# Performance work log

Hardware: AMD Instinct MI355X
Metric: run time of the kernel (lower is better)

Reference implementation:

```python
import jax, jax.numpy as jnp
import numpy as np

N_FEATURES = 7
N_SETS = 2
N_RULES = N_SETS ** N_FEATURES  # 128
BATCH = 65536


def setup_inputs() -> dict:
    key = jax.random.key(0)
    ks = jax.random.split(key, 7)
    centres = jnp.tile(jnp.linspace(-1.5, 1.5, N_SETS)[None, :], (N_FEATURES, 1))
    x = jax.random.normal(ks[0], (BATCH, N_FEATURES), jnp.float32)
    mu_gauss = centres + 0.1 * jax.random.normal(ks[1], centres.shape, jnp.float32)
    sigma_gauss = jnp.full((N_FEATURES, N_SETS), 0.8, jnp.float32)
    trap_a = centres - 1.2 + 0.05 * jax.random.normal(ks[2], centres.shape, jnp.float32)
    trap_b = centres - 0.4 + 0.05 * jax.random.normal(ks[3], centres.shape, jnp.float32)
    trap_c = centres + 0.4 + 0.05 * jax.random.normal(ks[4], centres.shape, jnp.float32)
    trap_d = centres + 1.2 + 0.05 * jax.random.normal(ks[5], centres.shape, jnp.float32)
    mf_mix = jnp.array(0.0, jnp.float32)
    t_norm_weight = jnp.array(0.0, jnp.float32)
    consequent = 0.01 * jax.random.normal(ks[6], (N_RULES, N_FEATURES + 1), jnp.float32)
    # itertools.product(range(S), repeat=F) ordering == np.indices row-major order
    rule_indices = jnp.asarray(
        np.indices((N_SETS,) * N_FEATURES).reshape(N_FEATURES, -1).T, jnp.int32
    )  # (N_RULES, N_FEATURES)
    return {
        "x": x, "mu_gauss": mu_gauss, "sigma_gauss": sigma_gauss,
        "trap_a": trap_a, "trap_b": trap_b, "trap_c": trap_c, "trap_d": trap_d,
        "mf_mix": mf_mix, "t_norm_weight": t_norm_weight,
        "consequent": consequent, "rule_indices": rule_indices,
    }


def reference(x, mu_gauss, sigma_gauss, trap_a, trap_b, trap_c, trap_d,
              mf_mix, t_norm_weight, consequent, rule_indices):
    B = x.shape[0]
    xe = x[..., None]  # (B, F, 1)
    # Gaussian MF
    sig = jnp.clip(sigma_gauss, 1e-6, None)
    gauss = jnp.exp(-(xe - mu_gauss) ** 2 / (2.0 * sig ** 2))  # (B, F, S)
    # Trapezoid MF with soft-sorted params a<b<=c<d
    params = jnp.sort(jnp.stack([trap_a, trap_b, trap_c, trap_d], axis=-1), axis=-1)
    a, b, c, d = params[..., 0], params[..., 1], params[..., 2], params[..., 3]
    left = jnp.clip((xe - a) / (b - a + 1e-6), 0.0, 1.0)
    flat = ((xe >= b) & (xe <= c)).astype(x.dtype)
    right = jnp.clip((d - xe) / (d - c + 1e-6), 0.0, 1.0)
    trap = jnp.maximum(jnp.minimum(left, right), flat)  # (B, F, S)
    # MF blend
    alpha = jax.nn.sigmoid(mf_mix)
    mem = alpha * gauss + (1.0 - alpha) * trap  # (B, F, S)
    # Rule gather: for each feature i, pick mem[:, i, rule_indices[:, i]]
    feat_idx = jnp.arange(N_FEATURES)[:, None]               # (F, 1)
    gathered = mem[:, feat_idx, rule_indices.T]              # (B, F, R)
    # Learnable t-norm: blend of product and min
    w = jax.nn.sigmoid(t_norm_weight)
    firing = w * jnp.prod(gathered, axis=1) + (1.0 - w) * jnp.min(gathered, axis=1)  # (B, R)
    norm_firing = firing / (jnp.sum(firing, axis=1, keepdims=True) + 1e-8)
    # TSK consequent: x_aug @ consequent^T
    x_aug = jnp.concatenate([jnp.ones((B, 1), x.dtype), x], axis=1)  # (B, F+1)
    rule_out = x_aug @ consequent.T                                  # (B, R)
    out = jnp.sum(norm_firing * rule_out, axis=1, keepdims=True)     # (B, 1)
    return (out, norm_firing, mem)
```

## Files before the change

### kernel.cpp

```cpp
#include <hip/hip_runtime.h>

#define NF 7
#define NR 128
#define ROWS 32

__global__ __launch_bounds__(256) void anfis_kernel(
    const float* __restrict__ x,
    const float* __restrict__ mu_g,  const float* __restrict__ sig_g,
    const float* __restrict__ ta, const float* __restrict__ tb,
    const float* __restrict__ tc, const float* __restrict__ td,
    const float* __restrict__ mf_mix, const float* __restrict__ tnw,
    const float* __restrict__ consequent,
    const int*   __restrict__ rule_idx,
    float* __restrict__ out,
    float* __restrict__ nf_out,
    float* __restrict__ mem_out,
    int nrows)
{
    __shared__ float s_x[ROWS][8];
    __shared__ float s_mem[ROWS][16];
    __shared__ unsigned int s_mask32[32];

    const int tid  = threadIdx.x;
    const int base = blockIdx.x * ROWS;

    if (tid < NR) {
        int m = 0;
        #pragma unroll
        for (int i = 0; i < NF; ++i)
            if (rule_idx[tid * NF + i] != 0) m |= (1 << i);
        ((unsigned char*)s_mask32)[tid] = (unsigned char)m;
    }

    const float alpha = 1.0f / (1.0f + __expf(-mf_mix[0]));
    const float w     = 1.0f / (1.0f + __expf(-tnw[0]));
    const float a1 = 1.0f - alpha, w1 = 1.0f - w;

    {
        const int j   = tid & 15;
        const int r16 = tid >> 4;

        float mu_j = 0.f, i2s2 = 0.f, q0 = 0.f, q1 = 0.f, q2 = 0.f, q3 = 0.f;
        float invL = 0.f, invR = 0.f;
        if (j < 14) {
            mu_j = mu_g[j];
            float sg = fmaxf(sig_g[j], 1e-6f);
            i2s2 = 1.0f / (2.0f * sg * sg);
            float p0 = ta[j], p1 = tb[j], p2 = tc[j], p3 = td[j];
            float lo, hi;
            lo = fminf(p0, p1); hi = fmaxf(p0, p1); p0 = lo; p1 = hi;
            lo = fminf(p2, p3); hi = fmaxf(p2, p3); p2 = lo; p3 = hi;
            lo = fminf(p0, p2); hi = fmaxf(p0, p2); p0 = lo; p2 = hi;
            lo = fminf(p1, p3); hi = fmaxf(p1, p3); p1 = lo; p3 = hi;
            lo = fminf(p1, p2); hi = fmaxf(p1, p2); p1 = lo; p2 = hi;
            q0 = p0; q1 = p1; q2 = p2; q3 = p3;
            invL = 1.0f / (p1 - p0 + 1e-6f);
            invR = 1.0f / (p3 - p2 + 1e-6f);
        }

        #pragma unroll
        for (int h = 0; h < 2; ++h) {
            const int rl  = r16 + 16 * h;
            const int row = base + rl;
            const bool live = (row < nrows);
            if (j < 14) {
                const float xi = live ? x[row * NF + (j >> 1)] : 0.0f;
                const float dm = xi - mu_j;
                const float gauss = __expf(-(dm * dm) * i2s2);
                float left = (xi - q0) * invL;
                left = fminf(fmaxf(left, 0.f), 1.f);
                const float flat = (xi >= q1 && xi <= q2) ? 1.f : 0.f;
                float right = (q3 - xi) * invR;
                right = fminf(fmaxf(right, 0.f), 1.f);
                const float trap = fmaxf(fminf(left, right), flat);
                const float m = fmaf(alpha, gauss, a1 * trap);
                s_mem[rl][j] = m;
                if (live) mem_out[row * 14 + j] = m;
                if ((j & 1) == 0) s_x[rl][1 + (j >> 1)] = xi;
            } else if (j == 15) {
                s_x[rl][0] = 1.0f;
            }
        }
    }
    __syncthreads();

    const int g  = tid >> 5;
    const int jj = tid & 31;
    const unsigned int pk = s_mask32[jj];
    const int r0 = 4 * jj;
    const float4* __restrict__ cq = (const float4*)consequent;

    #pragma unroll
    for (int it = 0; it < 4; ++it) {
        const int rl  = g + 8 * it;
        const int row = base + rl;
        const bool live = (row < nrows);

        const float4 xa0 = *(const float4*)&s_x[rl][0];
        const float4 xa1 = *(const float4*)&s_x[rl][4];
        const float4 mA = *(const float4*)&s_mem[rl][0];
        const float4 mB = *(const float4*)&s_mem[rl][4];
        const float4 mC = *(const float4*)&s_mem[rl][8];
        const float2 mD = *(const float2*)&s_mem[rl][12];

        const float mlo[7] = {mA.x, mA.z, mB.x, mB.z, mC.x, mC.z, mD.x};
        const float mhi[7] = {mA.y, mA.w, mB.y, mB.w, mC.y, mC.w, mD.y};

        const unsigned int m0 = pk & 0xffu;
        float p0 = (m0 & 1u)  ? mhi[0] : mlo[0];
        float p1 = (m0 & 2u)  ? mhi[1] : mlo[1];
        float p2 = (m0 & 4u)  ? mhi[2] : mlo[2];
        float p3 = (m0 & 8u)  ? mhi[3] : mlo[3];
        float p4 = (m0 & 16u) ? mhi[4] : mlo[4];
        const float P5 = ((p0 * p1) * (p2 * p3)) * p4;
        const float M5 = fminf(fminf(fminf(p0, p1), fminf(p2, p3)), p4);

        float f[4];
        float S = 0.f, dot = 0.f;
        #pragma unroll
        for (int k = 0; k < 4; ++k) {
            const unsigned int mk = pk >> (8 * k);
            const float g5 = (mk & 0x20u) ? mhi[5] : mlo[5];
            const float g6 = (mk & 0x40u) ? mhi[6] : mlo[6];
            const float prod = P5 * (g5 * g6);
            const float mn   = fminf(M5, fminf(g5, g6));
            const float fr   = fmaf(w, prod, w1 * mn);

            const int r = r0 + k;
            const float4 c0 = cq[2 * r];
            const float4 c1 = cq[2 * r + 1];
            float ro = c0.x * xa0.x;
            ro = fmaf(c0.y, xa0.y, ro);
            ro = fmaf(c0.z, xa0.z, ro);
            ro = fmaf(c0.w, xa0.w, ro);
            ro = fmaf(c1.x, xa1.x, ro);
            ro = fmaf(c1.y, xa1.y, ro);
            ro = fmaf(c1.z, xa1.z, ro);
            ro = fmaf(c1.w, xa1.w, ro);

            f[k] = fr;
            S += fr;
            dot = fmaf(fr, ro, dot);
        }

        #pragma unroll
        for (int off = 1; off < 32; off <<= 1) {
            S   += __shfl_xor(S, off, 64);
            dot += __shfl_xor(dot, off, 64);
        }
        const float invS = 1.0f / (S + 1e-8f);

        if (live) {
            float4 nf4;
            nf4.x = f[0] * invS;
            nf4.y = f[1] * invS;
            nf4.z = f[2] * invS;
            nf4.w = f[3] * invS;
            *(float4*)&nf_out[(size_t)row * NR + r0] = nf4;
            if (jj == 0) out[row] = dot * invS;
        }
    }
}

extern "C" void kernel_launch(void* const* d_in, const int* in_sizes, int n_in,
                              void* d_out, int out_size, void* d_ws, size_t ws_size,
                              hipStream_t stream) {
    const float* x     = (const float*)d_in[0];
    const float* mu_g  = (const float*)d_in[1];
    const float* sig_g = (const float*)d_in[2];
    const float* ta    = (const float*)d_in[3];
    const float* tb    = (const float*)d_in[4];
    const float* tc    = (const float*)d_in[5];
    const float* td    = (const float*)d_in[6];
    const float* mfm   = (const float*)d_in[7];
    const float* tnw   = (const float*)d_in[8];
    const float* cons  = (const float*)d_in[9];
    const int*   ridx  = (const int*)d_in[10];

    const int nrows = in_sizes[0] / NF;

    float* out     = (float*)d_out;
    float* nf_out  = out + nrows;
    float* mem_out = nf_out + (size_t)nrows * NR;

    const int grid = (nrows + ROWS - 1) / ROWS;
    anfis_kernel<<<grid, 256, 0, stream>>>(x, mu_g, sig_g, ta, tb, tc, td,
                                           mfm, tnw, cons, ridx,
                                           out, nf_out, mem_out, nrows);
}
```

Baseline: 115.7 us.

## Double rows per block, hoist consequent loads into registers, use nontemporal stores

Doubles the rows handled per block from 32 to 64, which halves the grid and spreads the per-block setup work (rule mask decoding, parameter sorting, sigmoid) over more rows. Each thread now loads its 8 consequent float4 values into registers once instead of reloading them on every row iteration. The output writes for mem and norm_firing become nontemporal stores to reduce cache pollution on a write-heavy kernel. The costs are more registers per thread and fewer blocks available to fill the GPU.

```diff
diff --git a/kernel.cpp b/kernel.cpp
--- a/kernel.cpp
+++ b/kernel.cpp
@@ -2,7 +2,10 @@
 
 #define NF 7
 #define NR 128
-#define ROWS 32
+#define ROWS 64
+#define CITERS 8
+
+typedef float v4f __attribute__((ext_vector_type(4)));
 
 __global__ __launch_bounds__(256) void anfis_kernel(
     const float* __restrict__ x,
@@ -59,7 +62,7 @@
         }
 
         #pragma unroll
-        for (int h = 0; h < 2; ++h) {
+        for (int h = 0; h < 4; ++h) {
             const int rl  = r16 + 16 * h;
             const int row = base + rl;
             const bool live = (row < nrows);
@@ -75,7 +78,7 @@
                 const float trap = fmaxf(fminf(left, right), flat);
                 const float m = fmaf(alpha, gauss, a1 * trap);
                 s_mem[rl][j] = m;
-                if (live) mem_out[row * 14 + j] = m;
+                if (live) __builtin_nontemporal_store(m, &mem_out[row * 14 + j]);
                 if ((j & 1) == 0) s_x[rl][1 + (j >> 1)] = xi;
             } else if (j == 15) {
                 s_x[rl][0] = 1.0f;
@@ -86,12 +89,18 @@
 
     const int g  = tid >> 5;
     const int jj = tid & 31;
-    const unsigned int pk = s_mask32[jj];
+    const unsigned int msks = s_mask32[jj];
     const int r0 = 4 * jj;
     const float4* __restrict__ cq = (const float4*)consequent;
 
+    float4 c[8];
     #pragma unroll
-    for (int it = 0; it < 4; ++it) {
+    for (int k = 0; k < 8; ++k) c[k] = cq[2 * r0 + k];
+
+    const unsigned int m0 = msks & 0xffu;
+
+    #pragma unroll 2
+    for (int it = 0; it < CITERS; ++it) {
         const int rl  = g + 8 * it;
         const int row = base + rl;
         const bool live = (row < nrows);
@@ -103,15 +112,11 @@
         const float4 mC = *(const float4*)&s_mem[rl][8];
         const float2 mD = *(const float2*)&s_mem[rl][12];
 
-        const float mlo[7] = {mA.x, mA.z, mB.x, mB.z, mC.x, mC.z, mD.x};
-        const float mhi[7] = {mA.y, mA.w, mB.y, mB.w, mC.y, mC.w, mD.y};
-
-        const unsigned int m0 = pk & 0xffu;
-        float p0 = (m0 & 1u)  ? mhi[0] : mlo[0];
-        float p1 = (m0 & 2u)  ? mhi[1] : mlo[1];
-        float p2 = (m0 & 4u)  ? mhi[2] : mlo[2];
-        float p3 = (m0 & 8u)  ? mhi[3] : mlo[3];
-        float p4 = (m0 & 16u) ? mhi[4] : mlo[4];
+        const float p0 = (m0 & 1u)  ? mA.y : mA.x;
+        const float p1 = (m0 & 2u)  ? mA.w : mA.z;
+        const float p2 = (m0 & 4u)  ? mB.y : mB.x;
+        const float p3 = (m0 & 8u)  ? mB.w : mB.z;
+        const float p4 = (m0 & 16u) ? mC.y : mC.x;
         const float P5 = ((p0 * p1) * (p2 * p3)) * p4;
         const float M5 = fminf(fminf(fminf(p0, p1), fminf(p2, p3)), p4);
 
@@ -119,16 +124,15 @@
         float S = 0.f, dot = 0.f;
         #pragma unroll
         for (int k = 0; k < 4; ++k) {
-            const unsigned int mk = pk >> (8 * k);
-            const float g5 = (mk & 0x20u) ? mhi[5] : mlo[5];
-            const float g6 = (mk & 0x40u) ? mhi[6] : mlo[6];
+            const unsigned int mk = msks >> (8 * k);
+            const float g5 = (mk & 0x20u) ? mC.w : mC.z;
+            const float g6 = (mk & 0x40u) ? mD.y : mD.x;
             const float prod = P5 * (g5 * g6);
             const float mn   = fminf(M5, fminf(g5, g6));
             const float fr   = fmaf(w, prod, w1 * mn);
 
-            const int r = r0 + k;
-            const float4 c0 = cq[2 * r];
-            const float4 c1 = cq[2 * r + 1];
+            const float4 c0 = c[2 * k];
+            const float4 c1 = c[2 * k + 1];
             float ro = c0.x * xa0.x;
             ro = fmaf(c0.y, xa0.y, ro);
             ro = fmaf(c0.z, xa0.z, ro);
@@ -151,12 +155,12 @@
         const float invS = 1.0f / (S + 1e-8f);
 
         if (live) {
-            float4 nf4;
+            v4f nf4;
             nf4.x = f[0] * invS;
             nf4.y = f[1] * invS;
             nf4.z = f[2] * invS;
             nf4.w = f[3] * invS;
-            *(float4*)&nf_out[(size_t)row * NR + r0] = nf4;
+            __builtin_nontemporal_store(nf4, (v4f*)&nf_out[(size_t)row * NR + r0]);
             if (jj == 0) out[row] = dot * invS;
         }
     }
```

New measurement: 96.15 us. 1.2x faster.
